# Performance work log

Hardware: AMD Instinct MI355X
Metric: run time of the kernel (lower is better)

## Reference

```python
import jax, jax.numpy as jnp
import numpy as np
from jax import lax

K = 3          # kernel size
PAD = 1        # (K-1)//2
CIN = 256
COUT = 64
NSPLIT = CIN // COUT  # 4
EPS = 1e-5


def _conv2d(x, w, b):
    # x [B,C,H,W], w [O,I,K,K], b [O]
    y = lax.conv_general_dilated(x, w, (1, 1), [(PAD, PAD), (PAD, PAD)],
                                 dimension_numbers=("NCHW", "OIHW", "NCHW"))
    return y + b[None, :, None, None]


def _bilinear_sample(img, py, px):
    # img [C,H,W]; py,px [K2,H,W] absolute sample coords; zero outside borders
    H, W = img.shape[1], img.shape[2]
    y0 = jnp.floor(py)
    x0 = jnp.floor(px)
    wy1 = py - y0
    wx1 = px - x0
    wy0 = 1.0 - wy1
    wx0 = 1.0 - wx1

    def gather(yc, xc):
        valid = (yc >= 0) & (yc <= H - 1) & (xc >= 0) & (xc <= W - 1)
        yi = jnp.clip(yc, 0, H - 1).astype(jnp.int32)
        xi = jnp.clip(xc, 0, W - 1).astype(jnp.int32)
        v = img[:, yi, xi]  # [C,K2,H,W]
        return v * valid.astype(img.dtype)[None]

    return (gather(y0, x0) * (wy0 * wx0)[None]
            + gather(y0, x0 + 1.0) * (wy0 * wx1)[None]
            + gather(y0 + 1.0, x0) * (wy1 * wx0)[None]
            + gather(y0 + 1.0, x0 + 1.0) * (wy1 * wx1)[None])


def _deform_conv(x, offsets, w, b):
    # x [B,C,H,W]; offsets [B,2*K2,H,W] (torchvision layout: per kernel pt (dy,dx));
    # w [O,C,K,K]; b [O]
    B, C, H, W = x.shape
    K2 = K * K
    off = offsets.reshape(B, K2, 2, H, W)
    kh = jnp.arange(K, dtype=x.dtype)
    base_y = (jnp.arange(H, dtype=x.dtype)[None, :, None]
              + (kh[:, None] - PAD).repeat(K).reshape(K2, 1, 1))  # h + kh - pad
    base_x = (jnp.arange(W, dtype=x.dtype)[None, None, :]
              + jnp.tile(kh - PAD, K).reshape(K2, 1, 1))          # w + kw - pad
    py = base_y + off[:, :, 0]  # [B,K2,H,W]
    px = base_x + off[:, :, 1]
    sampled = jax.vmap(_bilinear_sample)(x, py, px)  # [B,C,K2,H,W]
    out = jnp.einsum("bckhw,ock->bohw", sampled, w.reshape(w.shape[0], C, K2))
    return out + b[None, :, None, None]


def setup_inputs() -> dict:
    key = jax.random.key(0)
    ks = jax.random.split(key, 10)
    B, H, W = 8, 64, 64
    x = jax.random.normal(ks[0], (B, CIN, H, W), dtype=jnp.float32)
    bn_gamma = jax.random.normal(ks[1], (CIN,), dtype=jnp.float32) * 0.1 + 1.0
    bn_beta = jax.random.normal(ks[2], (CIN,), dtype=jnp.float32) * 0.1
    bn_mean = jax.random.normal(ks[3], (CIN,), dtype=jnp.float32) * 0.1
    bn_var = jax.random.uniform(ks[4], (CIN,), dtype=jnp.float32, minval=0.5, maxval=1.5)
    offset_w = jax.random.normal(ks[5], (NSPLIT, 2 * K * K, CIN, K, K), dtype=jnp.float32) * 0.02
    offset_b = jax.random.normal(ks[6], (NSPLIT, 2 * K * K), dtype=jnp.float32) * 0.02
    dconv_w = jax.random.normal(ks[7], (NSPLIT, COUT, COUT, K, K), dtype=jnp.float32) * 0.04
    dconv_b = jax.random.normal(ks[8], (NSPLIT, COUT), dtype=jnp.float32) * 0.02
    return {"x": x, "bn_gamma": bn_gamma, "bn_beta": bn_beta, "bn_mean": bn_mean,
            "bn_var": bn_var, "offset_w": offset_w, "offset_b": offset_b,
            "dconv_w": dconv_w, "dconv_b": dconv_b}


def reference(x, bn_gamma, bn_beta, bn_mean, bn_var, offset_w, offset_b, dconv_w, dconv_b):
    # BN (eval-mode running stats) + ReLU
    inv = lax.rsqrt(bn_var + EPS)
    h = jax.nn.relu((x - bn_mean[None, :, None, None]) * (bn_gamma * inv)[None, :, None, None]
                    + bn_beta[None, :, None, None])
    out = None
    for i in range(NSPLIT):
        offsets = _conv2d(h, offset_w[i], offset_b[i])               # [B,2K2,H,W]
        x_i = h[:, i * COUT:(i + 1) * COUT]                          # [B,COUT,H,W]
        y_i = _deform_conv(x_i, offsets, dconv_w[i], dconv_b[i])
        out = y_i if out is None else out + y_i
    return out
```

## Files before the change

kernel.cpp:

```cpp
#include <hip/hip_runtime.h>

#define KK 3
#define CIN 256
#define COUT 64
#define NSPLIT 4
#define BB 8
#define HH 64
#define WW 64
#define K2 9
#define OC 18
#define EPS 1e-5f

typedef __attribute__((ext_vector_type(8))) short bf16x8;
typedef __attribute__((ext_vector_type(4))) float f32x4;
typedef __attribute__((ext_vector_type(4))) unsigned int u32x4;

#define WS_BSUM  512
#define WS_HBF   1024
#define HBF_FLOATS (BB*HH*WW*CIN/2)
#define WS_OFFS  (WS_HBF + HBF_FLOATS)
#define OFFS_SIZE (BB*72*HH*WW)
#define WS_WDT   (WS_OFFS + OFFS_SIZE)
#define WS_WOB   (WS_WDT + NSPLIT*K2*COUT*COUT/2)
#define WOB_ELEMS (K2*80*CIN)
#define NBN_BLOCKS 2048
#define NWT_BLOCKS ((WOB_ELEMS + 255) / 256)

__device__ __host__ inline unsigned short f2bf(float f) {
    unsigned int u = __builtin_bit_cast(unsigned int, f);
    unsigned int r = (u + 0x7fffu + ((u >> 16) & 1u)) >> 16;
    return (unsigned short)r;
}
__device__ inline float bf2f(unsigned short u) {
    return __builtin_bit_cast(float, (unsigned int)u << 16);
}

__global__ __launch_bounds__(256) void prep_kernel(const float* __restrict__ x,
                                                   const float* __restrict__ g,
                                                   const float* __restrict__ be,
                                                   const float* __restrict__ mn,
                                                   const float* __restrict__ vr,
                                                   const float* __restrict__ dw,
                                                   const float* __restrict__ ow,
                                                   const float* __restrict__ db,
                                                   float* __restrict__ ws,
                                                   unsigned short* __restrict__ hbf) {
    if (blockIdx.x < NBN_BLOCKS) {
        __shared__ float tile[64 * 65];
        __shared__ float scl[64], bil[64];
        int bid = blockIdx.x;
        int cg = bid & 3;
        int y  = (bid >> 2) & 63;
        int b  = bid >> 8;
        int t = threadIdx.x;
        if (t < 64) {
            int c = cg * 64 + t;
            float inv = rsqrtf(vr[c] + EPS);
            float sc = g[c] * inv;
            scl[t] = sc;
            bil[t] = be[c] - mn[c] * sc;
        }
        __syncthreads();
        int lane = t & 63;
        int grp  = t >> 6;
        #pragma unroll
        for (int i = 0; i < 16; i++) {
            int cl = grp * 16 + i;
            int c  = cg * 64 + cl;
            float v = x[((b * CIN + c) * HH + y) * WW + lane];
            float h = fmaxf(fmaf(v, scl[cl], bil[cl]), 0.f);
            tile[cl * 65 + lane] = h;
        }
        __syncthreads();
        int cpair = t & 31;
        int pxg   = t >> 5;
        #pragma unroll
        for (int i = 0; i < 8; i++) {
            int px = pxg * 8 + i;
            unsigned int u0 = f2bf(tile[(cpair * 2) * 65 + px]);
            unsigned int u1 = f2bf(tile[(cpair * 2 + 1) * 65 + px]);
            *(unsigned int*)&hbf[((size_t)(b * HH + y) * WW + px) * CIN + cg * 64 + cpair * 2] =
                u0 | (u1 << 16);
        }
    } else {
        int tid = (blockIdx.x - NBN_BLOCKS) * 256 + threadIdx.x;
        if (blockIdx.x == NBN_BLOCKS && threadIdx.x < COUT) {
            float s = 0.f;
            for (int i = 0; i < NSPLIT; i++) s += db[i * COUT + threadIdx.x];
            ws[WS_BSUM + threadIdx.x] = s;
        }
        if (tid < NSPLIT * K2 * COUT * COUT) {
            int cin = tid & 63;
            int o = (tid >> 6) & 63;
            int k = (tid / 4096) % 9;
            int s = tid / 36864;
            ((unsigned short*)(ws + WS_WDT))[tid] = f2bf(dw[((s * COUT + o) * COUT + cin) * 9 + k]);
        }
        if (tid < WOB_ELEMS) {
            int cin = tid & 255;
            int sc = (tid >> 8) % 80;
            int k = tid / 20480;
            unsigned short v = 0;
            if (sc < 72) {
                int s = sc / 18, c = sc % 18;
                v = f2bf(ow[((s * OC + c) * CIN + cin) * 9 + k]);
            }
            ((unsigned short*)(ws + WS_WOB))[tid] = v;
        }
    }
}

__global__ __launch_bounds__(256) void offconv_kernel(const unsigned short* __restrict__ hbf,
                                                      const float* __restrict__ offb,
                                                      const unsigned short* __restrict__ woB,
                                                      float* __restrict__ offs_out) {
    __shared__ unsigned short wlds[80 * 264];
    int tid = threadIdx.x;
    int bid = blockIdx.x + 64 * blockIdx.y;
    int b = bid & 7;
    int y = bid >> 3;
    int w  = tid >> 6;
    int l  = tid & 63;
    int lm = l & 15, lk = l >> 4;
    int px = w * 16 + lm;

    f32x4 acc[5];
    #pragma unroll
    for (int nt = 0; nt < 5; nt++) {
        int sc = nt * 16 + lm;
        float ob = (sc < 72) ? offb[sc] : 0.f;
        acc[nt] = (f32x4){ob, ob, ob, ob};
    }
    const unsigned short* hb = hbf + (size_t)b * HH * WW * CIN;
    const bf16x8 zero = {};

    for (int k = 0; k < 9; k++) {
        int dy = k / 3 - 1, dx = k % 3 - 1;
        int ry = y + dy;
        if ((unsigned)ry >= (unsigned)HH) continue;
        __syncthreads();
        const unsigned short* src = woB + (size_t)k * 80 * 256;
        #pragma unroll
        for (int t = 0; t < 10; t++) {
            int idx = tid + t * 256;
            int sc = idx >> 5;
            int co = (idx & 31) * 8;
            *(bf16x8*)&wlds[sc * 264 + co] = *(const bf16x8*)&src[sc * 256 + co];
        }
        __syncthreads();

        int rx = px + dx;
        bool vx = (unsigned)rx < (unsigned)WW;
        const unsigned short* arow = hb + ((size_t)ry * WW + rx) * CIN + lk * 8;
        #pragma unroll
        for (int kt = 0; kt < 8; kt++) {
            bf16x8 a = vx ? *(const bf16x8*)(arow + kt * 32) : zero;
            #pragma unroll
            for (int nt = 0; nt < 5; nt++) {
                bf16x8 bb = *(const bf16x8*)&wlds[(nt * 16 + lm) * 264 + kt * 32 + lk * 8];
                acc[nt] = __builtin_amdgcn_mfma_f32_16x16x32_bf16(a, bb, acc[nt], 0, 0, 0);
            }
        }
    }

    #pragma unroll
    for (int nt = 0; nt < 5; nt++) {
        int sc = nt * 16 + lm;
        if (sc < 72) {
            float4 v = {acc[nt][0], acc[nt][1], acc[nt][2], acc[nt][3]};
            *(float4*)&offs_out[((size_t)(b * 72 + sc) * HH + y) * WW + w * 16 + lk * 4] = v;
        }
    }
}

#define RGN 18432
__global__ __launch_bounds__(512, 4) void deform_kernel(const unsigned short* __restrict__ hbf,
                                                        const float* __restrict__ offp,
                                                        const unsigned short* __restrict__ wdT,
                                                        const float* __restrict__ bsum,
                                                        float* __restrict__ out) {
    __shared__ __align__(16) char lds[2][RGN];

    int tid = threadIdx.x;
    int bid = blockIdx.x + 64 * blockIdx.y;
    int b = bid & 7;
    int y = bid >> 3;

    int h  = tid >> 8;
    int t8 = tid & 255;
    int l  = tid & 63;
    int w4 = t8 >> 6;
    int lm = l & 15;
    int lk = l >> 4;
    int pA = t8 >> 2;
    int cA = t8 & 3;
    int sub = l >> 3;
    int chq = l & 7;

    char* half_ = lds[h];
    char* vbufB = half_;
    char* wbufB = half_ + 8192;
    int2* tbl2  = (int2*)(half_ + 16384);

    f32x4 acc[4];
    #pragma unroll
    for (int nt = 0; nt < 4; nt++) {
        float bs = h ? 0.f : bsum[nt * 16 + lm];
        acc[nt] = (f32x4){bs, bs, bs, bs};
    }

    const unsigned short* hb = hbf + (size_t)b * HH * WW * CIN;
    const float* offbase = offp + ((size_t)(b * 72 + 2 * h * 18) * HH + y) * WW + pA;

    float offy_c = offbase[0];
    float offx_c = offbase[HH * WW];

    for (int it = 0; it < 2 * K2; ++it) {
        int sl = it >= K2;
        int s  = 2 * h + sl;
        int k  = it - sl * K2;

        float offy_n = 0.f, offx_n = 0.f;
        if (it + 1 < 2 * K2) {
            int sl2 = (it + 1) >= K2;
            int k2  = (it + 1) - sl2 * K2;
            const float* oa = offbase + (size_t)(sl2 * 18 + 2 * k2) * (HH * WW);
            offy_n = oa[0];
            offx_n = oa[HH * WW];
        }

        const unsigned short* wsrc = wdT + (size_t)((s * 9 + k) * 64) * 64;
        bf16x8 wr0 = *(const bf16x8*)(wsrc + t8 * 16);
        bf16x8 wr1 = *(const bf16x8*)(wsrc + t8 * 16 + 8);

        {
            int dy = k / 3 - 1, dx = k % 3 - 1;
            float py  = (float)(y + dy) + offy_c;
            float px_ = (float)(pA + dx) + offx_c;
            float y0f = floorf(py), x0f = floorf(px_);
            float wy1 = py - y0f, wx1 = px_ - x0f;
            int yt = (int)y0f + (cA >> 1);
            int xt = (int)x0f + (cA & 1);
            float wt = ((cA >> 1) ? wy1 : 1.f - wy1) * ((cA & 1) ? wx1 : 1.f - wx1);
            bool valid = (yt >= 0) && (yt < HH) && (xt >= 0) && (xt < WW);
            wt = valid ? wt : 0.f;
            int yi = min(max(yt, 0), HH - 1);
            int xi = min(max(xt, 0), WW - 1);
            tbl2[pA * 4 + cA] = (int2){yi * WW + xi, __builtin_bit_cast(int, wt)};
        }
        __syncthreads();

        {
            int pg0 = w4 * 16 + sub;
            int pg1 = pg0 + 8;
            float v0[8], v1[8];
            #pragma unroll
            for (int j = 0; j < 8; j++) { v0[j] = 0.f; v1[j] = 0.f; }
            const unsigned short* sb = hb + s * COUT + chq * 8;
            #pragma unroll
            for (int c = 0; c < 4; c++) {
                int2 t0 = tbl2[pg0 * 4 + c];
                int2 t1 = tbl2[pg1 * 4 + c];
                bf16x8 d0 = *(const bf16x8*)(sb + (size_t)t0.x * CIN);
                bf16x8 d1 = *(const bf16x8*)(sb + (size_t)t1.x * CIN);
                float w0 = __builtin_bit_cast(float, t0.y);
                float w1 = __builtin_bit_cast(float, t1.y);
                #pragma unroll
                for (int j = 0; j < 8; j++) {
                    v0[j] = fmaf(w0, bf2f((unsigned short)d0[j]), v0[j]);
                    v1[j] = fmaf(w1, bf2f((unsigned short)d1[j]), v1[j]);
                }
            }
            u32x4 q0, q1;
            #pragma unroll
            for (int j = 0; j < 4; j++) {
                q0[j] = (unsigned)f2bf(v0[2 * j]) | ((unsigned)f2bf(v0[2 * j + 1]) << 16);
                q1[j] = (unsigned)f2bf(v1[2 * j]) | ((unsigned)f2bf(v1[2 * j + 1]) << 16);
            }
            *(u32x4*)(vbufB + pg0 * 128 + ((chq * 16) ^ ((pg0 & 7) << 4))) = q0;
            *(u32x4*)(vbufB + pg1 * 128 + ((chq * 16) ^ ((pg1 & 7) << 4))) = q1;
        }
        {
            int wo = t8 >> 2, wq = t8 & 3;
            int sw = (wo & 7) << 4;
            *(bf16x8*)(wbufB + wo * 128 + ((wq * 32) ^ sw))      = wr0;
            *(bf16x8*)(wbufB + wo * 128 + ((wq * 32 + 16) ^ sw)) = wr1;
        }
        __syncthreads();

        {
            int aswz = (lm & 7) << 4;
            #pragma unroll
            for (int ks = 0; ks < 2; ks++) {
                bf16x8 a = *(const bf16x8*)(vbufB + (w4 * 16 + lm) * 128 +
                                            ((ks * 64 + lk * 16) ^ aswz));
                #pragma unroll
                for (int nt = 0; nt < 4; nt++) {
                    bf16x8 bb = *(const bf16x8*)(wbufB + (nt * 16 + lm) * 128 +
                                                 ((ks * 64 + lk * 16) ^ aswz));
                    acc[nt] = __builtin_amdgcn_mfma_f32_16x16x32_bf16(a, bb, acc[nt], 0, 0, 0);
                }
            }
        }

        offy_c = offy_n;
        offx_c = offx_n;
    }

    __syncthreads();
    float* outT = (float*)half_;
    #pragma unroll
    for (int nt = 0; nt < 4; nt++) {
        *(f32x4*)(&outT[(nt * 16 + lm) * 68 + w4 * 16 + lk * 4]) = acc[nt];
    }
    __syncthreads();
    {
        const float* o0 = (const float*)lds[0];
        const float* o1 = (const float*)lds[1];
        int o = tid >> 3, xp = (tid & 7) * 8;
        float* dst = out + (((size_t)(b * COUT + o)) * HH + y) * WW + xp;
        #pragma unroll
        for (int q = 0; q < 2; q++) {
            float4 a = *(const float4*)(&o0[o * 68 + xp + q * 4]);
            float4 c = *(const float4*)(&o1[o * 68 + xp + q * 4]);
            float4 rr = {a.x + c.x, a.y + c.y, a.z + c.z, a.w + c.w};
            *(float4*)(dst + q * 4) = rr;
        }
    }
}

extern "C" void kernel_launch(void* const* d_in, const int* in_sizes, int n_in,
                              void* d_out, int out_size, void* d_ws, size_t ws_size,
                              hipStream_t stream) {
    const float* x        = (const float*)d_in[0];
    const float* bn_gamma = (const float*)d_in[1];
    const float* bn_beta  = (const float*)d_in[2];
    const float* bn_mean  = (const float*)d_in[3];
    const float* bn_var   = (const float*)d_in[4];
    const float* offset_w = (const float*)d_in[5];
    const float* offset_b = (const float*)d_in[6];
    const float* dconv_w  = (const float*)d_in[7];
    const float* dconv_b  = (const float*)d_in[8];
    float* out = (float*)d_out;
    float* ws  = (float*)d_ws;

    unsigned short* hbf = (unsigned short*)(ws + WS_HBF);

    prep_kernel<<<NBN_BLOCKS + NWT_BLOCKS, 256, 0, stream>>>(x, bn_gamma, bn_beta, bn_mean,
                                                             bn_var, dconv_w, offset_w,
                                                             dconv_b, ws, hbf);
    offconv_kernel<<<dim3(64, 8), 256, 0, stream>>>(hbf, offset_b,
                                                    (const unsigned short*)(ws + WS_WOB),
                                                    ws + WS_OFFS);
    deform_kernel<<<dim3(64, 8), 512, 0, stream>>>(hbf, ws + WS_OFFS,
                                                   (const unsigned short*)(ws + WS_WDT),
                                                   ws + WS_BSUM, out);
}
```

Baseline: 86.04 us.

## Software-pipeline deformable gather with double-buffered tables and register prefetch

Restructures the deform kernel loop so the bilinear sample table for the next kernel point is built, and its gathered bf16 rows loaded into registers, one iteration ahead. The global gather latency then overlaps with the current iteration's MFMA work. Gather mapping also changes so each thread loads all four corners for one pixel and 16 channels, instead of splitting pixels across lanes. LDS per block half grows from 18 KB to 28 KB and the prefetched data raises register pressure, which may reduce occupancy at 4 blocks per CU.

```diff
diff --git a/kernel.cpp b/kernel.cpp
--- a/kernel.cpp
+++ b/kernel.cpp
@@ -10,6 +10,7 @@
 #define K2 9
 #define OC 18
 #define EPS 1e-5f
+#define HW (HH*WW)
 
 typedef __attribute__((ext_vector_type(8))) short bf16x8;
 typedef __attribute__((ext_vector_type(4))) float f32x4;
@@ -173,7 +174,7 @@
     }
 }
 
-#define RGN 18432
+#define RGN 28672
 __global__ __launch_bounds__(512, 4) void deform_kernel(const unsigned short* __restrict__ hbf,
                                                         const float* __restrict__ offp,
                                                         const unsigned short* __restrict__ wdT,
@@ -194,13 +195,16 @@
     int lk = l >> 4;
     int pA = t8 >> 2;
     int cA = t8 & 3;
-    int sub = l >> 3;
-    int chq = l & 7;
+    int gpx = t8 & 63;
+    int gcq = t8 >> 6;
+    int gsw = (gpx & 7) << 4;
 
     char* half_ = lds[h];
-    char* vbufB = half_;
-    char* wbufB = half_ + 8192;
-    int2* tbl2  = (int2*)(half_ + 16384);
+    char* vb0   = half_;
+    char* vb1   = half_ + 8192;
+    char* wbufB = half_ + 16384;
+    int2* tb0   = (int2*)(half_ + 24576);
+    int2* tb1   = (int2*)(half_ + 26624);
 
     f32x4 acc[4];
     #pragma unroll
@@ -212,31 +216,61 @@
     const unsigned short* hb = hbf + (size_t)b * HH * WW * CIN;
     const float* offbase = offp + ((size_t)(b * 72 + 2 * h * 18) * HH + y) * WW + pA;
 
-    float offy_c = offbase[0];
-    float offx_c = offbase[HH * WW];
-
-    for (int it = 0; it < 2 * K2; ++it) {
-        int sl = it >= K2;
+    char* vcur = vb0; char* vnxt = vb1;
+    int2* tcur = tb0; int2* tnxt = tb1;
+
+    {
+        float offy0 = offbase[0];
+        float offx0 = offbase[HW];
+        float py  = (float)(y - 1) + offy0;
+        float px_ = (float)(pA - 1) + offx0;
+        float y0f = floorf(py), x0f = floorf(px_);
+        float wy1 = py - y0f, wx1 = px_ - x0f;
+        int yt = (int)y0f + (cA >> 1);
+        int xt = (int)x0f + (cA & 1);
+        float wt = ((cA >> 1) ? wy1 : 1.f - wy1) * ((cA & 1) ? wx1 : 1.f - wx1);
+        bool valid = (yt >= 0) && (yt < HH) && (xt >= 0) && (xt < WW);
+        wt = valid ? wt : 0.f;
+        int yi = min(max(yt, 0), HH - 1);
+        int xi = min(max(xt, 0), WW - 1);
+        tcur[pA * 4 + cA] = (int2){yi * WW + xi, __builtin_bit_cast(int, wt)};
+    }
+    float offy_a = offbase[2 * HW];
+    float offx_a = offbase[3 * HW];
+    __syncthreads();
+
+    bf16x8 dA[4], dB[4];
+    float wtc[4];
+    {
+        const unsigned short* sb = hb + (2 * h) * COUT + gcq * 16;
+        int4 p01 = *(const int4*)&tcur[gpx * 4 + 0];
+        int4 p23 = *(const int4*)&tcur[gpx * 4 + 2];
+        wtc[0] = __builtin_bit_cast(float, p01.y);
+        wtc[1] = __builtin_bit_cast(float, p01.w);
+        wtc[2] = __builtin_bit_cast(float, p23.y);
+        wtc[3] = __builtin_bit_cast(float, p23.w);
+        const unsigned short* s0 = sb + (size_t)p01.x * CIN;
+        const unsigned short* s1 = sb + (size_t)p01.z * CIN;
+        const unsigned short* s2 = sb + (size_t)p23.x * CIN;
+        const unsigned short* s3 = sb + (size_t)p23.z * CIN;
+        dA[0] = *(const bf16x8*)s0; dB[0] = *(const bf16x8*)(s0 + 8);
+        dA[1] = *(const bf16x8*)s1; dB[1] = *(const bf16x8*)(s1 + 8);
+        dA[2] = *(const bf16x8*)s2; dB[2] = *(const bf16x8*)(s2 + 8);
+        dA[3] = *(const bf16x8*)s3; dB[3] = *(const bf16x8*)(s3 + 8);
+    }
+
+    for (int i = 0; i < 18; ++i) {
+        int sl = i >= 9;
         int s  = 2 * h + sl;
-        int k  = it - sl * K2;
-
-        float offy_n = 0.f, offx_n = 0.f;
-        if (it + 1 < 2 * K2) {
-            int sl2 = (it + 1) >= K2;
-            int k2  = (it + 1) - sl2 * K2;
-            const float* oa = offbase + (size_t)(sl2 * 18 + 2 * k2) * (HH * WW);
-            offy_n = oa[0];
-            offx_n = oa[HH * WW];
-        }
-
-        const unsigned short* wsrc = wdT + (size_t)((s * 9 + k) * 64) * 64;
-        bf16x8 wr0 = *(const bf16x8*)(wsrc + t8 * 16);
-        bf16x8 wr1 = *(const bf16x8*)(wsrc + t8 * 16 + 8);
-
-        {
-            int dy = k / 3 - 1, dx = k % 3 - 1;
-            float py  = (float)(y + dy) + offy_c;
-            float px_ = (float)(pA + dx) + offx_c;
+        int k  = i - sl * 9;
+
+        if (i < 17) {
+            int i1 = i + 1;
+            int sl1 = i1 >= 9;
+            int k1 = i1 - sl1 * 9;
+            int dy = k1 / 3 - 1, dx = k1 % 3 - 1;
+            float py  = (float)(y + dy) + offy_a;
+            float px_ = (float)(pA + dx) + offx_a;
             float y0f = floorf(py), x0f = floorf(px_);
             float wy1 = py - y0f, wx1 = px_ - x0f;
             int yt = (int)y0f + (cA >> 1);
@@ -246,39 +280,43 @@
             wt = valid ? wt : 0.f;
             int yi = min(max(yt, 0), HH - 1);
             int xi = min(max(xt, 0), WW - 1);
-            tbl2[pA * 4 + cA] = (int2){yi * WW + xi, __builtin_bit_cast(int, wt)};
-        }
+            tnxt[pA * 4 + cA] = (int2){yi * WW + xi, __builtin_bit_cast(int, wt)};
+            if (i < 16) {
+                int i2 = i + 2;
+                int sl2 = i2 >= 9;
+                int k2 = i2 - sl2 * 9;
+                int sc2 = sl2 * 18 + 2 * k2;
+                offy_a = offbase[(size_t)sc2 * HW];
+                offx_a = offbase[(size_t)(sc2 + 1) * HW];
+            }
+        }
+        const unsigned short* wsrc = wdT + (size_t)((s * 9 + k) * 64) * 64;
+        bf16x8 wr0 = *(const bf16x8*)(wsrc + t8 * 16);
+        bf16x8 wr1 = *(const bf16x8*)(wsrc + t8 * 16 + 8);
+
         __syncthreads();
 
         {
-            int pg0 = w4 * 16 + sub;
-            int pg1 = pg0 + 8;
-            float v0[8], v1[8];
+            float v[16];
             #pragma unroll
-            for (int j = 0; j < 8; j++) { v0[j] = 0.f; v1[j] = 0.f; }
-            const unsigned short* sb = hb + s * COUT + chq * 8;
+            for (int j = 0; j < 16; j++) v[j] = 0.f;
             #pragma unroll
             for (int c = 0; c < 4; c++) {
-                int2 t0 = tbl2[pg0 * 4 + c];
-                int2 t1 = tbl2[pg1 * 4 + c];
-                bf16x8 d0 = *(const bf16x8*)(sb + (size_t)t0.x * CIN);
-                bf16x8 d1 = *(const bf16x8*)(sb + (size_t)t1.x * CIN);
-                float w0 = __builtin_bit_cast(float, t0.y);
-                float w1 = __builtin_bit_cast(float, t1.y);
+                float w_ = wtc[c];
                 #pragma unroll
                 for (int j = 0; j < 8; j++) {
-                    v0[j] = fmaf(w0, bf2f((unsigned short)d0[j]), v0[j]);
-                    v1[j] = fmaf(w1, bf2f((unsigned short)d1[j]), v1[j]);
+                    v[j]     = fmaf(w_, bf2f((unsigned short)dA[c][j]), v[j]);
+                    v[j + 8] = fmaf(w_, bf2f((unsigned short)dB[c][j]), v[j + 8]);
                 }
             }
             u32x4 q0, q1;
             #pragma unroll
             for (int j = 0; j < 4; j++) {
-                q0[j] = (unsigned)f2bf(v0[2 * j]) | ((unsigned)f2bf(v0[2 * j + 1]) << 16);
-                q1[j] = (unsigned)f2bf(v1[2 * j]) | ((unsigned)f2bf(v1[2 * j + 1]) << 16);
-            }
-            *(u32x4*)(vbufB + pg0 * 128 + ((chq * 16) ^ ((pg0 & 7) << 4))) = q0;
-            *(u32x4*)(vbufB + pg1 * 128 + ((chq * 16) ^ ((pg1 & 7) << 4))) = q1;
+                q0[j] = (unsigned)f2bf(v[2 * j])     | ((unsigned)f2bf(v[2 * j + 1]) << 16);
+                q1[j] = (unsigned)f2bf(v[8 + 2 * j]) | ((unsigned)f2bf(v[9 + 2 * j]) << 16);
+            }
+            *(u32x4*)(vcur + gpx * 128 + ((gcq * 32) ^ gsw))      = q0;
+            *(u32x4*)(vcur + gpx * 128 + ((gcq * 32 + 16) ^ gsw)) = q1;
         }
         {
             int wo = t8 >> 2, wq = t8 & 3;
@@ -286,13 +324,31 @@
             *(bf16x8*)(wbufB + wo * 128 + ((wq * 32) ^ sw))      = wr0;
             *(bf16x8*)(wbufB + wo * 128 + ((wq * 32 + 16) ^ sw)) = wr1;
         }
+        if (i < 17) {
+            int s1 = 2 * h + ((i + 1) >= 9);
+            const unsigned short* sb = hb + s1 * COUT + gcq * 16;
+            int4 p01 = *(const int4*)&tnxt[gpx * 4 + 0];
+            int4 p23 = *(const int4*)&tnxt[gpx * 4 + 2];
+            wtc[0] = __builtin_bit_cast(float, p01.y);
+            wtc[1] = __builtin_bit_cast(float, p01.w);
+            wtc[2] = __builtin_bit_cast(float, p23.y);
+            wtc[3] = __builtin_bit_cast(float, p23.w);
+            const unsigned short* s0 = sb + (size_t)p01.x * CIN;
+            const unsigned short* s1p = sb + (size_t)p01.z * CIN;
+            const unsigned short* s2 = sb + (size_t)p23.x * CIN;
+            const unsigned short* s3 = sb + (size_t)p23.z * CIN;
+            dA[0] = *(const bf16x8*)s0;  dB[0] = *(const bf16x8*)(s0 + 8);
+            dA[1] = *(const bf16x8*)s1p; dB[1] = *(const bf16x8*)(s1p + 8);
+            dA[2] = *(const bf16x8*)s2;  dB[2] = *(const bf16x8*)(s2 + 8);
+            dA[3] = *(const bf16x8*)s3;  dB[3] = *(const bf16x8*)(s3 + 8);
+        }
         __syncthreads();
 
         {
             int aswz = (lm & 7) << 4;
             #pragma unroll
             for (int ks = 0; ks < 2; ks++) {
-                bf16x8 a = *(const bf16x8*)(vbufB + (w4 * 16 + lm) * 128 +
+                bf16x8 a = *(const bf16x8*)(vcur + (w4 * 16 + lm) * 128 +
                                             ((ks * 64 + lk * 16) ^ aswz));
                 #pragma unroll
                 for (int nt = 0; nt < 4; nt++) {
@@ -303,8 +359,8 @@
             }
         }
 
-        offy_c = offy_n;
-        offx_c = offx_n;
+        { char* t = vcur; vcur = vnxt; vnxt = t; }
+        { int2* t = tcur; tcur = tnxt; tnxt = t; }
     }
 
     __syncthreads();
```

New measurement: 120.6 us. 40.2% more time.

## Split deform kernel rows into half-row tiles to double grid and occupancy

Applied to the files above, without the earlier changes.

The deform kernel now handles 32 output pixels per block instead of a full 64-pixel row. This doubles the grid to 1024 blocks, shrinks shared memory per block, and raises the launch-bounds occupancy hint from 4 to 6. The four waves are rearranged into a 2x2 M/N split for the MFMA stage, and each thread gathers one pixel group instead of two. The aim is more parallelism and better latency hiding for the gather-heavy loop. The cost is that each weight tile load is amortised over fewer pixels, so per-output weight traffic and synchronisation overhead rise.

```diff
diff --git a/kernel.cpp b/kernel.cpp
--- a/kernel.cpp
+++ b/kernel.cpp
@@ -10,6 +10,7 @@
 #define K2 9
 #define OC 18
 #define EPS 1e-5f
+#define HW (HH*WW)
 
 typedef __attribute__((ext_vector_type(8))) short bf16x8;
 typedef __attribute__((ext_vector_type(4))) float f32x4;
@@ -173,8 +174,8 @@
     }
 }
 
-#define RGN 18432
-__global__ __launch_bounds__(512, 4) void deform_kernel(const unsigned short* __restrict__ hbf,
+#define RGN 13312
+__global__ __launch_bounds__(512, 6) void deform_kernel(const unsigned short* __restrict__ hbf,
                                                         const float* __restrict__ offp,
                                                         const unsigned short* __restrict__ wdT,
                                                         const float* __restrict__ bsum,
@@ -182,38 +183,43 @@
     __shared__ __align__(16) char lds[2][RGN];
 
     int tid = threadIdx.x;
-    int bid = blockIdx.x + 64 * blockIdx.y;
-    int b = bid & 7;
-    int y = bid >> 3;
+    int bid = blockIdx.x + 128 * blockIdx.y;
+    int b  = bid & 7;
+    int r  = bid >> 3;
+    int y  = r >> 1;
+    int xh = r & 1;
 
     int h  = tid >> 8;
     int t8 = tid & 255;
     int l  = tid & 63;
     int w4 = t8 >> 6;
+    int wm = w4 >> 1;
+    int wn = w4 & 1;
     int lm = l & 15;
     int lk = l >> 4;
-    int pA = t8 >> 2;
+    int pA = (t8 & 127) >> 2;
     int cA = t8 & 3;
-    int sub = l >> 3;
-    int chq = l & 7;
+    int gp  = t8 >> 3;
+    int chq = t8 & 7;
+    int gsw = (gp & 7) << 4;
 
     char* half_ = lds[h];
     char* vbufB = half_;
-    char* wbufB = half_ + 8192;
-    int2* tbl2  = (int2*)(half_ + 16384);
-
-    f32x4 acc[4];
+    char* wbufB = half_ + 4096;
+    int2* tbl2  = (int2*)(half_ + 12288);
+
+    f32x4 acc[2];
     #pragma unroll
-    for (int nt = 0; nt < 4; nt++) {
-        float bs = h ? 0.f : bsum[nt * 16 + lm];
+    for (int nt = 0; nt < 2; nt++) {
+        float bs = h ? 0.f : bsum[wn * 32 + nt * 16 + lm];
         acc[nt] = (f32x4){bs, bs, bs, bs};
     }
 
     const unsigned short* hb = hbf + (size_t)b * HH * WW * CIN;
-    const float* offbase = offp + ((size_t)(b * 72 + 2 * h * 18) * HH + y) * WW + pA;
+    const float* offbase = offp + ((size_t)(b * 72 + 2 * h * 18) * HH + y) * WW + xh * 32 + pA;
 
     float offy_c = offbase[0];
-    float offx_c = offbase[HH * WW];
+    float offx_c = offbase[HW];
 
     for (int it = 0; it < 2 * K2; ++it) {
         int sl = it >= K2;
@@ -224,9 +230,9 @@
         if (it + 1 < 2 * K2) {
             int sl2 = (it + 1) >= K2;
             int k2  = (it + 1) - sl2 * K2;
-            const float* oa = offbase + (size_t)(sl2 * 18 + 2 * k2) * (HH * WW);
+            const float* oa = offbase + (size_t)(sl2 * 18 + 2 * k2) * HW;
             offy_n = oa[0];
-            offx_n = oa[HH * WW];
+            offx_n = oa[HW];
         }
 
         const unsigned short* wsrc = wdT + (size_t)((s * 9 + k) * 64) * 64;
@@ -236,7 +242,7 @@
         {
             int dy = k / 3 - 1, dx = k % 3 - 1;
             float py  = (float)(y + dy) + offy_c;
-            float px_ = (float)(pA + dx) + offx_c;
+            float px_ = (float)(xh * 32 + pA + dx) + offx_c;
             float y0f = floorf(py), x0f = floorf(px_);
             float wy1 = py - y0f, wx1 = px_ - x0f;
             int yt = (int)y0f + (cA >> 1);
@@ -251,34 +257,26 @@
         __syncthreads();
 
         {
-            int pg0 = w4 * 16 + sub;
-            int pg1 = pg0 + 8;
-            float v0[8], v1[8];
-            #pragma unroll
-            for (int j = 0; j < 8; j++) { v0[j] = 0.f; v1[j] = 0.f; }
+            float v[8];
+            #pragma unroll
+            for (int j = 0; j < 8; j++) v[j] = 0.f;
             const unsigned short* sb = hb + s * COUT + chq * 8;
             #pragma unroll
             for (int c = 0; c < 4; c++) {
-                int2 t0 = tbl2[pg0 * 4 + c];
-                int2 t1 = tbl2[pg1 * 4 + c];
+                int2 t0 = tbl2[gp * 4 + c];
                 bf16x8 d0 = *(const bf16x8*)(sb + (size_t)t0.x * CIN);
-                bf16x8 d1 = *(const bf16x8*)(sb + (size_t)t1.x * CIN);
                 float w0 = __builtin_bit_cast(float, t0.y);
-                float w1 = __builtin_bit_cast(float, t1.y);
                 #pragma unroll
                 for (int j = 0; j < 8; j++) {
-                    v0[j] = fmaf(w0, bf2f((unsigned short)d0[j]), v0[j]);
-                    v1[j] = fmaf(w1, bf2f((unsigned short)d1[j]), v1[j]);
+                    v[j] = fmaf(w0, bf2f((unsigned short)d0[j]), v[j]);
                 }
             }
-            u32x4 q0, q1;
+            u32x4 q0;
             #pragma unroll
             for (int j = 0; j < 4; j++) {
-                q0[j] = (unsigned)f2bf(v0[2 * j]) | ((unsigned)f2bf(v0[2 * j + 1]) << 16);
-                q1[j] = (unsigned)f2bf(v1[2 * j]) | ((unsigned)f2bf(v1[2 * j + 1]) << 16);
-            }
-            *(u32x4*)(vbufB + pg0 * 128 + ((chq * 16) ^ ((pg0 & 7) << 4))) = q0;
-            *(u32x4*)(vbufB + pg1 * 128 + ((chq * 16) ^ ((pg1 & 7) << 4))) = q1;
+                q0[j] = (unsigned)f2bf(v[2 * j]) | ((unsigned)f2bf(v[2 * j + 1]) << 16);
+            }
+            *(u32x4*)(vbufB + gp * 128 + ((chq * 16) ^ gsw)) = q0;
         }
         {
             int wo = t8 >> 2, wq = t8 & 3;
@@ -292,11 +290,11 @@
             int aswz = (lm & 7) << 4;
             #pragma unroll
             for (int ks = 0; ks < 2; ks++) {
-                bf16x8 a = *(const bf16x8*)(vbufB + (w4 * 16 + lm) * 128 +
+                bf16x8 a = *(const bf16x8*)(vbufB + (wm * 16 + lm) * 128 +
                                             ((ks * 64 + lk * 16) ^ aswz));
                 #pragma unroll
-                for (int nt = 0; nt < 4; nt++) {
-                    bf16x8 bb = *(const bf16x8*)(wbufB + (nt * 16 + lm) * 128 +
+                for (int nt = 0; nt < 2; nt++) {
+                    bf16x8 bb = *(const bf16x8*)(wbufB + (wn * 32 + nt * 16 + lm) * 128 +
                                                  ((ks * 64 + lk * 16) ^ aswz));
                     acc[nt] = __builtin_amdgcn_mfma_f32_16x16x32_bf16(a, bb, acc[nt], 0, 0, 0);
                 }
@@ -310,22 +308,18 @@
     __syncthreads();
     float* outT = (float*)half_;
     #pragma unroll
-    for (int nt = 0; nt < 4; nt++) {
-        *(f32x4*)(&outT[(nt * 16 + lm) * 68 + w4 * 16 + lk * 4]) = acc[nt];
+    for (int nt = 0; nt < 2; nt++) {
+        *(f32x4*)(&outT[(wn * 32 + nt * 16 + lm) * 36 + wm * 16 + lk * 4]) = acc[nt];
     }
     __syncthreads();
     {
         const float* o0 = (const float*)lds[0];
         const float* o1 = (const float*)lds[1];
-        int o = tid >> 3, xp = (tid & 7) * 8;
-        float* dst = out + (((size_t)(b * COUT + o)) * HH + y) * WW + xp;
-        #pragma unroll
-        for (int q = 0; q < 2; q++) {
-            float4 a = *(const float4*)(&o0[o * 68 + xp + q * 4]);
-            float4 c = *(const float4*)(&o1[o * 68 + xp + q * 4]);
-            float4 rr = {a.x + c.x, a.y + c.y, a.z + c.z, a.w + c.w};
-            *(float4*)(dst + q * 4) = rr;
-        }
+        int o = tid >> 3, xq = (tid & 7) * 4;
+        float4 a = *(const float4*)(&o0[o * 36 + xq]);
+        float4 c = *(const float4*)(&o1[o * 36 + xq]);
+        float4 rr = {a.x + c.x, a.y + c.y, a.z + c.z, a.w + c.w};
+        *(float4*)(out + (((size_t)(b * COUT + o)) * HH + y) * WW + xh * 32 + xq) = rr;
     }
 }
 
@@ -352,7 +346,7 @@
     offconv_kernel<<<dim3(64, 8), 256, 0, stream>>>(hbf, offset_b,
                                                     (const unsigned short*)(ws + WS_WOB),
                                                     ws + WS_OFFS);
-    deform_kernel<<<dim3(64, 8), 512, 0, stream>>>(hbf, ws + WS_OFFS,
-                                                   (const unsigned short*)(ws + WS_WDT),
-                                                   ws + WS_BSUM, out);
-}
+    deform_kernel<<<dim3(128, 8), 512, 0, stream>>>(hbf, ws + WS_OFFS,
+                                                    (const unsigned short*)(ws + WS_WDT),
+                                                    ws + WS_BSUM, out);
+}
```

Result: slower. 100.2 us (+16.5%).

## Split deform kernel across four split-groups per block with 1024 threads

Applied to the files above, without the earlier changes.

The deform kernel now assigns each of the four channel splits to its own 256-thread group inside a 1024-thread block, instead of two groups each looping over two splits. Each group runs 9 kernel-point iterations instead of 18, and the final reduction sums four LDS partial tiles. This aims to shorten the serial loop per block and raise parallelism, with 512 blocks total. The cost is larger blocks with more LDS per block (72KB) and register pressure under launch_bounds(1024), which may lower occupancy.

```diff
diff --git a/kernel.cpp b/kernel.cpp
--- a/kernel.cpp
+++ b/kernel.cpp
@@ -10,6 +10,7 @@
 #define K2 9
 #define OC 18
 #define EPS 1e-5f
+#define HW (HH*WW)
 
 typedef __attribute__((ext_vector_type(8))) short bf16x8;
 typedef __attribute__((ext_vector_type(4))) float f32x4;
@@ -174,19 +175,19 @@
 }
 
 #define RGN 18432
-__global__ __launch_bounds__(512, 4) void deform_kernel(const unsigned short* __restrict__ hbf,
-                                                        const float* __restrict__ offp,
-                                                        const unsigned short* __restrict__ wdT,
-                                                        const float* __restrict__ bsum,
-                                                        float* __restrict__ out) {
-    __shared__ __align__(16) char lds[2][RGN];
+__global__ __launch_bounds__(1024, 8) void deform_kernel(const unsigned short* __restrict__ hbf,
+                                                         const float* __restrict__ offp,
+                                                         const unsigned short* __restrict__ wdT,
+                                                         const float* __restrict__ bsum,
+                                                         float* __restrict__ out) {
+    __shared__ __align__(16) char lds[4][RGN];
 
     int tid = threadIdx.x;
     int bid = blockIdx.x + 64 * blockIdx.y;
     int b = bid & 7;
     int y = bid >> 3;
 
-    int h  = tid >> 8;
+    int q  = tid >> 8;
     int t8 = tid & 255;
     int l  = tid & 63;
     int w4 = t8 >> 6;
@@ -197,39 +198,33 @@
     int sub = l >> 3;
     int chq = l & 7;
 
-    char* half_ = lds[h];
-    char* vbufB = half_;
-    char* wbufB = half_ + 8192;
-    int2* tbl2  = (int2*)(half_ + 16384);
+    char* qr    = lds[q];
+    char* vbufB = qr;
+    char* wbufB = qr + 8192;
+    int2* tbl2  = (int2*)(qr + 16384);
 
     f32x4 acc[4];
     #pragma unroll
     for (int nt = 0; nt < 4; nt++) {
-        float bs = h ? 0.f : bsum[nt * 16 + lm];
+        float bs = q ? 0.f : bsum[nt * 16 + lm];
         acc[nt] = (f32x4){bs, bs, bs, bs};
     }
 
     const unsigned short* hb = hbf + (size_t)b * HH * WW * CIN;
-    const float* offbase = offp + ((size_t)(b * 72 + 2 * h * 18) * HH + y) * WW + pA;
+    const float* offbase = offp + ((size_t)(b * 72 + q * 18) * HH + y) * WW + pA;
 
     float offy_c = offbase[0];
-    float offx_c = offbase[HH * WW];
-
-    for (int it = 0; it < 2 * K2; ++it) {
-        int sl = it >= K2;
-        int s  = 2 * h + sl;
-        int k  = it - sl * K2;
-
+    float offx_c = offbase[HW];
+
+    for (int k = 0; k < K2; ++k) {
         float offy_n = 0.f, offx_n = 0.f;
-        if (it + 1 < 2 * K2) {
-            int sl2 = (it + 1) >= K2;
-            int k2  = (it + 1) - sl2 * K2;
-            const float* oa = offbase + (size_t)(sl2 * 18 + 2 * k2) * (HH * WW);
+        if (k + 1 < K2) {
+            const float* oa = offbase + (size_t)(2 * (k + 1)) * HW;
             offy_n = oa[0];
-            offx_n = oa[HH * WW];
-        }
-
-        const unsigned short* wsrc = wdT + (size_t)((s * 9 + k) * 64) * 64;
+            offx_n = oa[HW];
+        }
+
+        const unsigned short* wsrc = wdT + (size_t)((q * 9 + k) * 64) * 64;
         bf16x8 wr0 = *(const bf16x8*)(wsrc + t8 * 16);
         bf16x8 wr1 = *(const bf16x8*)(wsrc + t8 * 16 + 8);
 
@@ -256,7 +251,7 @@
             float v0[8], v1[8];
             #pragma unroll
             for (int j = 0; j < 8; j++) { v0[j] = 0.f; v1[j] = 0.f; }
-            const unsigned short* sb = hb + s * COUT + chq * 8;
+            const unsigned short* sb = hb + q * COUT + chq * 8;
             #pragma unroll
             for (int c = 0; c < 4; c++) {
                 int2 t0 = tbl2[pg0 * 4 + c];
@@ -308,24 +303,23 @@
     }
 
     __syncthreads();
-    float* outT = (float*)half_;
+    float* outT = (float*)qr;
     #pragma unroll
     for (int nt = 0; nt < 4; nt++) {
         *(f32x4*)(&outT[(nt * 16 + lm) * 68 + w4 * 16 + lk * 4]) = acc[nt];
     }
     __syncthreads();
     {
-        const float* o0 = (const float*)lds[0];
-        const float* o1 = (const float*)lds[1];
-        int o = tid >> 3, xp = (tid & 7) * 8;
-        float* dst = out + (((size_t)(b * COUT + o)) * HH + y) * WW + xp;
-        #pragma unroll
-        for (int q = 0; q < 2; q++) {
-            float4 a = *(const float4*)(&o0[o * 68 + xp + q * 4]);
-            float4 c = *(const float4*)(&o1[o * 68 + xp + q * 4]);
-            float4 rr = {a.x + c.x, a.y + c.y, a.z + c.z, a.w + c.w};
-            *(float4*)(dst + q * 4) = rr;
-        }
+        int o = tid >> 4, xp = (tid & 15) * 4;
+        float4 a0 = *(const float4*)(&((const float*)lds[0])[o * 68 + xp]);
+        float4 a1 = *(const float4*)(&((const float*)lds[1])[o * 68 + xp]);
+        float4 a2 = *(const float4*)(&((const float*)lds[2])[o * 68 + xp]);
+        float4 a3 = *(const float4*)(&((const float*)lds[3])[o * 68 + xp]);
+        float4 rr = {a0.x + a1.x + a2.x + a3.x,
+                     a0.y + a1.y + a2.y + a3.y,
+                     a0.z + a1.z + a2.z + a3.z,
+                     a0.w + a1.w + a2.w + a3.w};
+        *(float4*)(out + (((size_t)(b * COUT + o)) * HH + y) * WW + xp) = rr;
     }
 }
 
@@ -352,7 +346,7 @@
     offconv_kernel<<<dim3(64, 8), 256, 0, stream>>>(hbf, offset_b,
                                                     (const unsigned short*)(ws + WS_WOB),
                                                     ws + WS_OFFS);
-    deform_kernel<<<dim3(64, 8), 512, 0, stream>>>(hbf, ws + WS_OFFS,
-                                                   (const unsigned short*)(ws + WS_WDT),
-                                                   ws + WS_BSUM, out);
-}
+    deform_kernel<<<dim3(64, 8), 1024, 0, stream>>>(hbf, ws + WS_OFFS,
+                                                    (const unsigned short*)(ws + WS_WDT),
+                                                    ws + WS_BSUM, out);
+}
```

Result: slower. 195.4 us (+127.0%).
